# Kernel tuning notes

Measured on AMD Instinct MI355X. Metric: run time of the kernel, lower is better.

The kernel has to match this reference:

```python
import jax, jax.numpy as jnp
import numpy as np

B = 8192          # number of analysis windows
N = 4096          # window_size (power of 2, matches radix-2 Cooley-Tukey)


def setup_inputs() -> dict:
    key = jax.random.key(0)
    x = jax.random.normal(key, (B, N), dtype=jnp.float32)
    return {"x": x}


def reference(x):
    """Power spectrum |F(k)|^2 per window.

    The original module implements an exact radix-2 DIT Cooley-Tukey FFT
    (bit-reversal permutation + log2(N) butterfly stages with twiddle
    factors exp(-2*pi*i*k/N)) and returns re^2 + im^2. That is exactly the
    unnormalized DFT, so the clean/efficient faithful form is jnp.fft.fft
    followed by squared magnitude, batched over the leading axis.
    """
    f = jnp.fft.fft(x.astype(jnp.complex64), axis=-1)  # [B, N] complex
    return (jnp.real(f) ** 2 + jnp.imag(f) ** 2).astype(x.dtype)  # [B, N]
```

## Files before the change

kernel.cpp:

```cpp
#include <hip/hip_runtime.h>
#include <math.h>

#define FFT_N   4096
#define NT      256
#define PHYS(i) ((i) + ((i) >> 4))
#define LDS_SZ  (FFT_N + FFT_N / 16)

__device__ __forceinline__ float2 cadd(float2 a, float2 b) { return make_float2(a.x + b.x, a.y + b.y); }
__device__ __forceinline__ float2 csub(float2 a, float2 b) { return make_float2(a.x - b.x, a.y - b.y); }
__device__ __forceinline__ float2 cmul(float2 a, float2 b) { return make_float2(a.x * b.x - a.y * b.y, a.x * b.y + a.y * b.x); }

__device__ __forceinline__ void dft4(float2& a, float2& b, float2& c, float2& d) {
    float2 t0 = cadd(a, c);
    float2 t1 = csub(a, c);
    float2 t2 = cadd(b, d);
    float2 t3 = make_float2(b.y - d.y, d.x - b.x);
    a = cadd(t0, t2);
    b = cadd(t1, t3);
    c = csub(t0, t2);
    d = csub(t1, t3);
}

__device__ __forceinline__ void dft16(float2 v[16]) {
    #pragma unroll
    for (int r1 = 0; r1 < 4; ++r1)
        dft4(v[r1], v[r1 + 4], v[r1 + 8], v[r1 + 12]);

    const float C1 = 0.92387953251128675613f;
    const float S1 = 0.38268343236508977173f;
    const float R2 = 0.70710678118654752440f;
    v[5]  = cmul(v[5],  make_float2( C1, -S1));
    v[9]  = cmul(v[9],  make_float2( R2, -R2));
    v[13] = cmul(v[13], make_float2( S1, -C1));
    v[6]  = cmul(v[6],  make_float2( R2, -R2));
    v[10] = make_float2(v[10].y, -v[10].x);
    v[14] = cmul(v[14], make_float2(-R2, -R2));
    v[7]  = cmul(v[7],  make_float2( S1, -C1));
    v[11] = cmul(v[11], make_float2(-R2, -R2));
    v[15] = cmul(v[15], make_float2(-C1,  S1));
    #pragma unroll
    for (int q1 = 0; q1 < 4; ++q1)
        dft4(v[4 * q1], v[4 * q1 + 1], v[4 * q1 + 2], v[4 * q1 + 3]);
}

template <int M, bool TW>
__device__ __forceinline__ void store_stage(float2* buf, int tid, float2 v[16]) {
    const int j = tid / M;
    const int k = tid % M;
    const int obase = j * 16 * M + k;
    if (TW) {
        float sn, cs;
        __sincosf((float)j * (-6.28318530717958647692f * (float)M / (float)FFT_N), &sn, &cs);
        const float2 w1 = make_float2(cs, sn);
        float2 wq = w1;
        buf[PHYS(obase)] = v[0];
        #pragma unroll
        for (int q = 1; q < 16; ++q) {
            const int reg = ((q & 3) << 2) | (q >> 2);
            buf[PHYS(obase + q * M)] = cmul(v[reg], wq);
            wq = cmul(wq, w1);
        }
    } else {
        #pragma unroll
        for (int q = 0; q < 16; ++q) {
            const int reg = ((q & 3) << 2) | (q >> 2);
            buf[PHYS(obase + q * M)] = v[reg];
        }
    }
}

__device__ __forceinline__ void load_stage(const float2* buf, int tid, float2 v[16]) {
    #pragma unroll
    for (int r = 0; r < 16; ++r) v[r] = buf[PHYS(tid + 256 * r)];
}

__global__ __launch_bounds__(NT) void spec_fft_kernel(const float* __restrict__ x,
                                                      float* __restrict__ out) {
    __shared__ float2 buf[LDS_SZ];
    const int tid = threadIdx.x;
    const size_t base = (size_t)blockIdx.x * (2 * FFT_N);
    const float* __restrict__ x1 = x + base + tid;
    const float* __restrict__ x2 = x + base + FFT_N + tid;

    float2 v[16];
    #pragma unroll
    for (int r = 0; r < 16; ++r)
        v[r] = make_float2(x1[256 * r], x2[256 * r]);

    dft16(v);
    store_stage<1, true>(buf, tid, v);
    __syncthreads();

    load_stage(buf, tid, v);
    __syncthreads();
    dft16(v);
    store_stage<16, true>(buf, tid, v);
    __syncthreads();

    load_stage(buf, tid, v);
    __syncthreads();
    dft16(v);
    store_stage<256, false>(buf, tid, v);
    __syncthreads();

    float* __restrict__ o1 = out + base;
    float* __restrict__ o2 = out + base + FFT_N;
    #pragma unroll
    for (int it = 0; it < 4; ++it) {
        int idx = tid + 256 * it;
        float4 r1, r2;
        #pragma unroll
        for (int c = 0; c < 4; ++c) {
            int k = 4 * idx + c;
            float2 zk = buf[PHYS(k)];
            float2 zn = buf[PHYS((FFT_N - k) & (FFT_N - 1))];
            float e1r = zk.x + zn.x, e1i = zk.y - zn.y;
            float e2r = zk.x - zn.x, e2i = zk.y + zn.y;
            (&r1.x)[c] = 0.25f * (e1r * e1r + e1i * e1i);
            (&r2.x)[c] = 0.25f * (e2r * e2r + e2i * e2i);
        }
        ((float4*)o1)[idx] = r1;
        ((float4*)o2)[idx] = r2;
    }
}

extern "C" void kernel_launch(void* const* d_in, const int* in_sizes, int n_in,
                              void* d_out, int out_size, void* d_ws, size_t ws_size,
                              hipStream_t stream) {
    const float* x = (const float*)d_in[0];
    float* out = (float*)d_out;
    const int B = in_sizes[0] / FFT_N;
    spec_fft_kernel<<<B / 2, NT, 0, stream>>>(x, out);
}
```

Baseline: 50.31 us.

## Switch FFT to four radix-8 stages with 512 threads per block

```diff
diff --git a/kernel.cpp b/kernel.cpp
--- a/kernel.cpp
+++ b/kernel.cpp
@@ -2,7 +2,7 @@
 #include <math.h>
 
 #define FFT_N   4096
-#define NT      256
+#define NT      512
 #define PHYS(i) ((i) + ((i) >> 4))
 #define LDS_SZ  (FFT_N + FFT_N / 16)
 
@@ -21,106 +21,101 @@
     d = csub(t1, t3);
 }
 
-__device__ __forceinline__ void dft16(float2 v[16]) {
+__device__ __forceinline__ void dft8(float2 v[8]) {
+    const float R2 = 0.70710678118654752440f;
+    float2 e0 = v[0], e1 = v[2], e2 = v[4], e3 = v[6];
+    float2 o0 = v[1], o1 = v[3], o2 = v[5], o3 = v[7];
+    dft4(e0, e1, e2, e3);
+    dft4(o0, o1, o2, o3);
+    o1 = make_float2(R2 * (o1.x + o1.y), R2 * (o1.y - o1.x));
+    o2 = make_float2(o2.y, -o2.x);
+    o3 = make_float2(R2 * (o3.y - o3.x), -R2 * (o3.x + o3.y));
+    v[0] = cadd(e0, o0); v[4] = csub(e0, o0);
+    v[1] = cadd(e1, o1); v[5] = csub(e1, o1);
+    v[2] = cadd(e2, o2); v[6] = csub(e2, o2);
+    v[3] = cadd(e3, o3); v[7] = csub(e3, o3);
+}
+
+__device__ __forceinline__ void load8(const float2* buf, int t, float2 v[8]) {
     #pragma unroll
-    for (int r1 = 0; r1 < 4; ++r1)
-        dft4(v[r1], v[r1 + 4], v[r1 + 8], v[r1 + 12]);
-
-    const float C1 = 0.92387953251128675613f;
-    const float S1 = 0.38268343236508977173f;
-    const float R2 = 0.70710678118654752440f;
-    v[5]  = cmul(v[5],  make_float2( C1, -S1));
-    v[9]  = cmul(v[9],  make_float2( R2, -R2));
-    v[13] = cmul(v[13], make_float2( S1, -C1));
-    v[6]  = cmul(v[6],  make_float2( R2, -R2));
-    v[10] = make_float2(v[10].y, -v[10].x);
-    v[14] = cmul(v[14], make_float2(-R2, -R2));
-    v[7]  = cmul(v[7],  make_float2( S1, -C1));
-    v[11] = cmul(v[11], make_float2(-R2, -R2));
-    v[15] = cmul(v[15], make_float2(-C1,  S1));
-    #pragma unroll
-    for (int q1 = 0; q1 < 4; ++q1)
-        dft4(v[4 * q1], v[4 * q1 + 1], v[4 * q1 + 2], v[4 * q1 + 3]);
+    for (int r = 0; r < 8; ++r) v[r] = buf[PHYS(t + 512 * r)];
 }
 
 template <int M, bool TW>
-__device__ __forceinline__ void store_stage(float2* buf, int tid, float2 v[16]) {
-    const int j = tid / M;
-    const int k = tid % M;
-    const int obase = j * 16 * M + k;
+__device__ __forceinline__ void store_stage8(float2* buf, int t, float2 v[8]) {
+    const int j = t / M;
+    const int k = t % M;
+    const int obase = j * 8 * M + k;
     if (TW) {
         float sn, cs;
         __sincosf((float)j * (-6.28318530717958647692f * (float)M / (float)FFT_N), &sn, &cs);
         const float2 w1 = make_float2(cs, sn);
-        float2 wq = w1;
-        buf[PHYS(obase)] = v[0];
-        #pragma unroll
-        for (int q = 1; q < 16; ++q) {
-            const int reg = ((q & 3) << 2) | (q >> 2);
-            buf[PHYS(obase + q * M)] = cmul(v[reg], wq);
-            wq = cmul(wq, w1);
-        }
+        const float2 w2 = cmul(w1, w1);
+        const float2 w3 = cmul(w2, w1);
+        const float2 w4 = cmul(w2, w2);
+        buf[PHYS(obase)]         = v[0];
+        buf[PHYS(obase + 1 * M)] = cmul(v[1], w1);
+        buf[PHYS(obase + 2 * M)] = cmul(v[2], w2);
+        buf[PHYS(obase + 3 * M)] = cmul(v[3], w3);
+        buf[PHYS(obase + 4 * M)] = cmul(v[4], w4);
+        buf[PHYS(obase + 5 * M)] = cmul(v[5], cmul(w4, w1));
+        buf[PHYS(obase + 6 * M)] = cmul(v[6], cmul(w4, w2));
+        buf[PHYS(obase + 7 * M)] = cmul(v[7], cmul(w4, w3));
     } else {
         #pragma unroll
-        for (int q = 0; q < 16; ++q) {
-            const int reg = ((q & 3) << 2) | (q >> 2);
-            buf[PHYS(obase + q * M)] = v[reg];
-        }
+        for (int q = 0; q < 8; ++q)
+            buf[PHYS(obase + q * M)] = v[q];
     }
 }
 
-__device__ __forceinline__ void load_stage(const float2* buf, int tid, float2 v[16]) {
+__global__ __launch_bounds__(NT, 8) void spec_fft_kernel(const float* __restrict__ x,
+                                                         float* __restrict__ out) {
+    __shared__ float2 buf[LDS_SZ];
+    const int t = threadIdx.x;
+    const size_t base = (size_t)blockIdx.x * (2 * FFT_N);
+    const float* __restrict__ x1 = x + base + t;
+    const float* __restrict__ x2 = x + base + FFT_N + t;
+
+    float2 v[8];
     #pragma unroll
-    for (int r = 0; r < 16; ++r) v[r] = buf[PHYS(tid + 256 * r)];
-}
+    for (int r = 0; r < 8; ++r)
+        v[r] = make_float2(x1[512 * r], x2[512 * r]);
 
-__global__ __launch_bounds__(NT) void spec_fft_kernel(const float* __restrict__ x,
-                                                      float* __restrict__ out) {
-    __shared__ float2 buf[LDS_SZ];
-    const int tid = threadIdx.x;
-    const size_t base = (size_t)blockIdx.x * (2 * FFT_N);
-    const float* __restrict__ x1 = x + base + tid;
-    const float* __restrict__ x2 = x + base + FFT_N + tid;
-
-    float2 v[16];
-    #pragma unroll
-    for (int r = 0; r < 16; ++r)
-        v[r] = make_float2(x1[256 * r], x2[256 * r]);
-
-    dft16(v);
-    store_stage<1, true>(buf, tid, v);
+    dft8(v);
+    store_stage8<1, true>(buf, t, v);
     __syncthreads();
 
-    load_stage(buf, tid, v);
+    load8(buf, t, v);
     __syncthreads();
-    dft16(v);
-    store_stage<16, true>(buf, tid, v);
+    dft8(v);
+    store_stage8<8, true>(buf, t, v);
     __syncthreads();
 
-    load_stage(buf, tid, v);
+    load8(buf, t, v);
     __syncthreads();
-    dft16(v);
-    store_stage<256, false>(buf, tid, v);
+    dft8(v);
+    store_stage8<64, true>(buf, t, v);
+    __syncthreads();
+
+    load8(buf, t, v);
+    __syncthreads();
+    dft8(v);
+    #pragma unroll
+    for (int q = 0; q < 8; ++q)
+        buf[PHYS(t + 512 * q)] = v[q];
     __syncthreads();
 
     float* __restrict__ o1 = out + base;
     float* __restrict__ o2 = out + base + FFT_N;
     #pragma unroll
-    for (int it = 0; it < 4; ++it) {
-        int idx = tid + 256 * it;
-        float4 r1, r2;
-        #pragma unroll
-        for (int c = 0; c < 4; ++c) {
-            int k = 4 * idx + c;
-            float2 zk = buf[PHYS(k)];
-            float2 zn = buf[PHYS((FFT_N - k) & (FFT_N - 1))];
-            float e1r = zk.x + zn.x, e1i = zk.y - zn.y;
-            float e2r = zk.x - zn.x, e2i = zk.y + zn.y;
-            (&r1.x)[c] = 0.25f * (e1r * e1r + e1i * e1i);
-            (&r2.x)[c] = 0.25f * (e2r * e2r + e2i * e2i);
-        }
-        ((float4*)o1)[idx] = r1;
-        ((float4*)o2)[idx] = r2;
+    for (int q = 0; q < 8; ++q) {
+        const int k = t + 512 * q;
+        float2 zk = v[q];
+        float2 zn = buf[PHYS((FFT_N - k) & (FFT_N - 1))];
+        float e1r = zk.x + zn.x, e1i = zk.y - zn.y;
+        float e2r = zk.x - zn.x, e2i = zk.y + zn.y;
+        __builtin_nontemporal_store(0.25f * (e1r * e1r + e1i * e1i), o1 + k);
+        __builtin_nontemporal_store(0.25f * (e2r * e2r + e2i * e2i), o2 + k);
     }
 }
 
```

Result: no change. 51.07 us (+1.5%).
